# Kernel tuning notes

Hardware: AMD Instinct MI355X
Metric: run time of the kernel (lower is better)

## Reference

```python
import jax, jax.numpy as jnp
import numpy as np

K = 32          # kneighbors
HEADS = 4       # Anchor_selfattention head_num
EPS = 1e-5      # BatchNorm eps


def bn(x, gamma, beta):
    # training-mode BatchNorm1d on channel-last tensor [B, M, C]:
    # stats over batch+spatial dims per channel, biased variance (torch behavior)
    m = jnp.mean(x, axis=(0, 1), keepdims=True)
    v = jnp.var(x, axis=(0, 1), keepdims=True)
    return gamma * (x - m) * jax.lax.rsqrt(v + EPS) + beta


def setup_inputs() -> dict:
    B, NA, NP, C, NRAW = 32, 4, 16384, 256, 32768
    key = jax.random.key(0)
    ks = jax.random.split(key, 12)
    s = 0.02
    return {
        "a_points": jax.random.normal(ks[0], (B, NA, 3), jnp.float32),
        "sa_x": jax.random.normal(ks[1], (B, NP, C), jnp.float32),
        "sa_xyz": jax.random.normal(ks[2], (B, NP, 3), jnp.float32),
        "xyz_raw": jax.random.normal(ks[3], (B, NRAW, 3), jnp.float32),
        # global_layer: Conv1d(3->C, bias=False) + BN(C)
        "g_W": jax.random.normal(ks[4], (C, 3), jnp.float32) * s,
        "g_gamma": jnp.ones((C,), jnp.float32),
        "g_beta": jnp.zeros((C,), jnp.float32),
        # attention: to_qkv Linear(C -> 3C, bias=False)
        "qkv_W": jax.random.normal(ks[5], (3 * C, C), jnp.float32) * s,
        # pos_embedding: Conv1d(3->C) + BN(C)
        "pos_W": jax.random.normal(ks[6], (C, 3), jnp.float32) * s,
        "pos_b": jnp.zeros((C,), jnp.float32),
        "pos_gamma": jnp.ones((C,), jnp.float32),
        "pos_beta": jnp.zeros((C,), jnp.float32),
        # res: Conv1d(C->C) + BN(C)
        "res_W": jax.random.normal(ks[7], (C, C), jnp.float32) * s,
        "res_b": jnp.zeros((C,), jnp.float32),
        "res_gamma": jnp.ones((C,), jnp.float32),
        "res_beta": jnp.zeros((C,), jnp.float32),
        # prob_head: Conv1d(2C -> 9, bias=False) + BN(9)
        "prob_W": jax.random.normal(ks[8], (9, 2 * C), jnp.float32) * s,
        "prob_gamma": jnp.ones((9,), jnp.float32),
        "prob_beta": jnp.zeros((9,), jnp.float32),
    }


def reference(a_points, sa_x, sa_xyz, xyz_raw,
              g_W, g_gamma, g_beta,
              qkv_W,
              pos_W, pos_b, pos_gamma, pos_beta,
              res_W, res_b, res_gamma, res_beta,
              prob_W, prob_gamma, prob_beta):
    B, NA, _ = a_points.shape
    C = sa_x.shape[-1]
    hd = C // HEADS

    # ---- knn_point: squared distances anchor->points, smallest-K indices ----
    # dist[b, a, n] = |a_points[b,a] - sa_xyz[b,n]|^2
    d = (-2.0 * jnp.einsum("bac,bnc->ban", a_points, sa_xyz)
         + jnp.sum(a_points ** 2, -1)[:, :, None]
         + jnp.sum(sa_xyz ** 2, -1)[:, None, :])
    _, idx = jax.lax.top_k(-d, K)                      # [B, NA, K]

    # ---- index_points gather + max-pool over neighbors ----
    local = jnp.take_along_axis(sa_x[:, None, :, :], idx[..., None], axis=2)  # [B,NA,K,C]
    local_feat = jnp.max(local, axis=2)                # [B, NA, C]

    # ---- Anchor self-attention ----
    gc = jnp.mean(a_points, axis=1, keepdims=True)
    rel = a_points - gc                                # [B, NA, 3]
    pos = bn(rel @ pos_W.T + pos_b, pos_gamma, pos_beta)   # [B, NA, C]

    qkv = local_feat @ qkv_W.T                         # [B, NA, 3C]
    q, k, v = jnp.split(qkv, 3, axis=-1)
    q, k, v = q + pos, k + pos, v + pos
    q = q.reshape(B, NA, HEADS, hd)
    k = k.reshape(B, NA, HEADS, hd)
    v = v.reshape(B, NA, HEADS, hd)
    attn = jnp.einsum("bmhd,bnhd->bhmn", q, k) / np.sqrt(hd).astype(np.float32)
    attn = jax.nn.softmax(attn, axis=-1)
    av = jnp.einsum("bhmn,bnhd->bmhd", attn, v).reshape(B, NA, C)
    res = bn(av @ res_W.T + res_b, res_gamma, res_beta)

    local_feat = local_feat + res                      # [B, NA, C]

    # ---- global branch ----
    gfeat = bn(a_points @ g_W.T, g_gamma, g_beta)      # [B, NA, C]
    gmax = jnp.max(gfeat, axis=1, keepdims=True)       # [B, 1, C]
    feat = jnp.concatenate(
        [local_feat, jnp.broadcast_to(gmax, (B, NA, C))], axis=-1)  # [B, NA, 2C]

    prob = bn(feat @ prob_W.T, prob_gamma, prob_beta)  # [B, NA, 9]
    return prob
```

## Files before the change

### kernel.cpp

```cpp
#include <hip/hip_runtime.h>
#include <math.h>

#define NPTS 16384
#define HALF 8192
#define NB   32
#define NA   4
#define NC   256
#define KNN  32
#define NROW 128
#define CAP  1024

#define OFF_LF      0
#define OFF_QKV     32768
#define OFF_RESLIN  131072
#define OFF_POSLIN  163840
#define OFF_POSST   196608
#define OFF_GLIN    197120
#define OFF_GST     229888
#define OFF_PROBLIN 230400
#define OFF_CAND    231552
#define OFF_CNT     247936

typedef unsigned long long ull;

__global__ __launch_bounds__(512) void knn_gather_kernel(
    const float* __restrict__ a_points, const float* __restrict__ sa_xyz,
    const float* __restrict__ sa_x,
    ull* __restrict__ cand, unsigned int* __restrict__ cnt,
    float* __restrict__ lf)
{
  const int blk  = blockIdx.x;
  const int row  = blk >> 1;
  const int half = blk & 1;
  const int b    = row >> 2;
  const int t    = threadIdx.x;

  __shared__ float s_T;
  __shared__ int   s_m;
  __shared__ int   s_winflag;
  __shared__ ull   s_cand[CAP];
  __shared__ ull   s64[64];
  __shared__ int   s_top[KNN];
  __shared__ float s_lf2[2][NC];
  float* smin = (float*)s_cand;

  const float ax = a_points[row*3 + 0];
  const float ay = a_points[row*3 + 1];
  const float az = a_points[row*3 + 2];
  const float* __restrict__ xyz = sa_xyz + (size_t)b * NPTS * 3 + (size_t)half * HALF * 3;

  float d[16];
#pragma unroll
  for (int j = 0; j < 16; ++j) {
    const int n = t + 512*j;
    const float dx = xyz[n*3+0] - ax;
    const float dy = xyz[n*3+1] - ay;
    const float dz = xyz[n*3+2] - az;
    d[j] = dx*dx + dy*dy + dz*dz;
  }
  float mn = d[0];
#pragma unroll
  for (int j = 1; j < 16; ++j) mn = fminf(mn, d[j]);
  if (t == 0) s_m = 0;
  smin[t] = mn;
  __syncthreads();

  if (t < 64) {
    unsigned v[8];
#pragma unroll
    for (int q = 0; q < 8; ++q) v[q] = __float_as_uint(smin[t + 64*q]);
    unsigned lo = 0u, hi = 0x7f7fffffu;
    while (lo < hi) {
      const unsigned mid = lo + ((hi - lo) >> 1);
      int c2 = 0;
#pragma unroll
      for (int q = 0; q < 8; ++q) c2 += (int)__popcll(__ballot(v[q] <= mid));
      if (c2 >= KNN) hi = mid; else lo = mid + 1;
    }
    if (t == 0) s_T = __uint_as_float(lo);
  }
  __syncthreads();
  const float T = s_T;

#pragma unroll
  for (int j = 0; j < 16; ++j) {
    if (d[j] <= T) {
      const int pos = atomicAdd(&s_m, 1);
      if (pos < CAP)
        s_cand[pos] = ((ull)__float_as_uint(d[j]) << 32) | (unsigned)(half*HALF + t + 512*j);
    }
  }
  __syncthreads();
  const int m = (s_m < CAP) ? s_m : CAP;

  for (int c2 = t; c2 < m; c2 += 512) {
    const ull me = s_cand[c2];
    int rank = 0;
    for (int j = 0; j < m; ++j) rank += (s_cand[j] < me);
    if (rank < KNN)
      __hip_atomic_store(&cand[(size_t)row*64 + half*KNN + rank], me,
                         __ATOMIC_RELAXED, __HIP_MEMORY_SCOPE_AGENT);
  }
  __syncthreads();

  if (t == 0) {
    const unsigned old = atomicAdd(&cnt[row], 1u);
    s_winflag = (((old + 1u) & 1u) == 0u);
  }
  __syncthreads();
  if (!s_winflag) return;

  if (t < 64)
    s64[t] = __hip_atomic_load(&cand[(size_t)row*64 + t],
                               __ATOMIC_RELAXED, __HIP_MEMORY_SCOPE_AGENT);
  __syncthreads();
  if (t < 64) {
    const ull me = s64[t];
    int rank = 0;
#pragma unroll
    for (int j = 0; j < 64; ++j) rank += (s64[j] < me);
    if (rank < KNN) s_top[rank] = (int)(unsigned)(me & 0xffffffffu);
  }
  __syncthreads();

  {
    const int c = t & 255, h = t >> 8;
    const float* __restrict__ xb = sa_x + (size_t)b * NPTS * NC;
    float acc = -3.0e38f;
#pragma unroll
    for (int r2 = 0; r2 < 16; ++r2)
      acc = fmaxf(acc, xb[(size_t)s_top[h*16 + r2] * NC + c]);
    s_lf2[h][c] = acc;
  }
  __syncthreads();
  if (t < NC)
    lf[(size_t)row * NC + t] = fmaxf(s_lf2[0][t], s_lf2[1][t]);
}

__global__ __launch_bounds__(256) void lin1_kernel(
    const float* __restrict__ lf, const float* __restrict__ qkv_W,
    const float* __restrict__ a_points,
    const float* __restrict__ pos_W, const float* __restrict__ pos_b,
    const float* __restrict__ g_W,
    float* __restrict__ qkv, float* __restrict__ pos_lin, float* __restrict__ pos_stats,
    float* __restrict__ g_lin, float* __restrict__ g_stats)
{
  const int blk = blockIdx.x;
  if (blk < 96) {
    const int r0 = (blk / 12) * 16;
    const int o0 = (blk % 12) * 64;
    const int ot = threadIdx.x & 63;
    const int rt = threadIdx.x >> 6;
    const int o  = o0 + ot;
    const float* __restrict__ wrow = qkv_W + (size_t)o * NC;
    const float* __restrict__ l0p  = lf + (size_t)(r0 + rt*4) * NC;
    float acc0 = 0.f, acc1 = 0.f, acc2 = 0.f, acc3 = 0.f;
    for (int c = 0; c < NC; c += 4) {
      const float4 w4 = *(const float4*)(wrow + c);
      const float4 l0 = *(const float4*)(l0p + c);
      const float4 l1 = *(const float4*)(l0p + NC + c);
      const float4 l2 = *(const float4*)(l0p + 2*NC + c);
      const float4 l3 = *(const float4*)(l0p + 3*NC + c);
      acc0 = fmaf(l0.x,w4.x,acc0); acc0 = fmaf(l0.y,w4.y,acc0); acc0 = fmaf(l0.z,w4.z,acc0); acc0 = fmaf(l0.w,w4.w,acc0);
      acc1 = fmaf(l1.x,w4.x,acc1); acc1 = fmaf(l1.y,w4.y,acc1); acc1 = fmaf(l1.z,w4.z,acc1); acc1 = fmaf(l1.w,w4.w,acc1);
      acc2 = fmaf(l2.x,w4.x,acc2); acc2 = fmaf(l2.y,w4.y,acc2); acc2 = fmaf(l2.z,w4.z,acc2); acc2 = fmaf(l2.w,w4.w,acc2);
      acc3 = fmaf(l3.x,w4.x,acc3); acc3 = fmaf(l3.y,w4.y,acc3); acc3 = fmaf(l3.z,w4.z,acc3); acc3 = fmaf(l3.w,w4.w,acc3);
    }
    const int r = r0 + rt*4;
    qkv[(size_t)(r+0)*768 + o] = acc0;
    qkv[(size_t)(r+1)*768 + o] = acc1;
    qkv[(size_t)(r+2)*768 + o] = acc2;
    qkv[(size_t)(r+3)*768 + o] = acc3;
  } else if (blk == 96) {
    __shared__ float apts[NROW*3];
    for (int i = threadIdx.x; i < NROW*3; i += 256) apts[i] = a_points[i];
    __syncthreads();
    const int c = threadIdx.x;
    const float w0 = pos_W[c*3+0], w1 = pos_W[c*3+1], w2 = pos_W[c*3+2];
    const float bb = pos_b[c];
    float sum = 0.f, sumsq = 0.f;
    for (int b = 0; b < NB; ++b) {
      float gx=0.f, gy=0.f, gz=0.f;
#pragma unroll
      for (int a = 0; a < NA; ++a) {
        gx += apts[(b*NA+a)*3+0];
        gy += apts[(b*NA+a)*3+1];
        gz += apts[(b*NA+a)*3+2];
      }
      gx *= 0.25f; gy *= 0.25f; gz *= 0.25f;
#pragma unroll
      for (int a = 0; a < NA; ++a) {
        const float v = (apts[(b*NA+a)*3+0]-gx)*w0
                      + (apts[(b*NA+a)*3+1]-gy)*w1
                      + (apts[(b*NA+a)*3+2]-gz)*w2 + bb;
        pos_lin[(b*NA+a)*NC + c] = v;
        sum += v; sumsq += v*v;
      }
    }
    pos_stats[c] = sum; pos_stats[NC + c] = sumsq;
  } else {
    __shared__ float apts[NROW*3];
    for (int i = threadIdx.x; i < NROW*3; i += 256) apts[i] = a_points[i];
    __syncthreads();
    const int c = threadIdx.x;
    const float w0 = g_W[c*3+0], w1 = g_W[c*3+1], w2 = g_W[c*3+2];
    float sum = 0.f, sumsq = 0.f;
    for (int r = 0; r < NROW; ++r) {
      const float v = apts[r*3+0]*w0 + apts[r*3+1]*w1 + apts[r*3+2]*w2;
      g_lin[r*NC + c] = v;
      sum += v; sumsq += v*v;
    }
    g_stats[c] = sum; g_stats[NC + c] = sumsq;
  }
}

__global__ __launch_bounds__(256) void attn_kernel(
    const float* __restrict__ qkv, const float* __restrict__ pos_lin,
    const float* __restrict__ pos_stats,
    const float* __restrict__ pos_gamma, const float* __restrict__ pos_beta,
    const float* __restrict__ res_W, const float* __restrict__ res_b,
    float* __restrict__ res_lin)
{
  const int b = blockIdx.x;
  const int t = threadIdx.x;
  __shared__ float av_s[NA][NC];
  const int c = t;
  const float pmean = pos_stats[c] * (1.0f/NROW);
  const float pvar  = pos_stats[NC + c] * (1.0f/NROW) - pmean*pmean;
  const float prstd = 1.0f / sqrtf(pvar + 1e-5f);
  const float pga = pos_gamma[c], pbe = pos_beta[c];

  float q[NA], k[NA], vv[NA];
#pragma unroll
  for (int a = 0; a < NA; ++a) {
    const int row = b*NA + a;
    const float p = pga * (pos_lin[(size_t)row*NC + c] - pmean) * prstd + pbe;
    q[a]  = qkv[(size_t)row*768 +       c] + p;
    k[a]  = qkv[(size_t)row*768 + 256 + c] + p;
    vv[a] = qkv[(size_t)row*768 + 512 + c] + p;
  }
  float s[NA][NA];
#pragma unroll
  for (int m = 0; m < NA; ++m) {
#pragma unroll
    for (int n = 0; n < NA; ++n) {
      float p = q[m]*k[n];
#pragma unroll
      for (int off = 1; off < 64; off <<= 1) p += __shfl_xor(p, off);
      s[m][n] = p * 0.125f;
    }
  }
#pragma unroll
  for (int m = 0; m < NA; ++m) {
    const float mx = fmaxf(fmaxf(s[m][0], s[m][1]), fmaxf(s[m][2], s[m][3]));
    const float e0 = expf(s[m][0]-mx), e1 = expf(s[m][1]-mx);
    const float e2 = expf(s[m][2]-mx), e3 = expf(s[m][3]-mx);
    const float inv = 1.0f / (e0+e1+e2+e3);
    av_s[m][c] = (e0*vv[0] + e1*vv[1] + e2*vv[2] + e3*vv[3]) * inv;
  }
  __syncthreads();

  const float* __restrict__ wrow = res_W + (size_t)c * NC;
  float r0=0.f, r1=0.f, r2=0.f, r3=0.f;
  for (int cc = 0; cc < NC; cc += 4) {
    const float4 w4 = *(const float4*)(wrow + cc);
    const float4 v0 = *(const float4*)&av_s[0][cc];
    const float4 v1 = *(const float4*)&av_s[1][cc];
    const float4 v2 = *(const float4*)&av_s[2][cc];
    const float4 v3 = *(const float4*)&av_s[3][cc];
    r0 = fmaf(v0.x,w4.x,r0); r0 = fmaf(v0.y,w4.y,r0); r0 = fmaf(v0.z,w4.z,r0); r0 = fmaf(v0.w,w4.w,r0);
    r1 = fmaf(v1.x,w4.x,r1); r1 = fmaf(v1.y,w4.y,r1); r1 = fmaf(v1.z,w4.z,r1); r1 = fmaf(v1.w,w4.w,r1);
    r2 = fmaf(v2.x,w4.x,r2); r2 = fmaf(v2.y,w4.y,r2); r2 = fmaf(v2.z,w4.z,r2); r2 = fmaf(v2.w,w4.w,r2);
    r3 = fmaf(v3.x,w4.x,r3); r3 = fmaf(v3.y,w4.y,r3); r3 = fmaf(v3.z,w4.z,r3); r3 = fmaf(v3.w,w4.w,r3);
  }
  const float bias = res_b[c];
  res_lin[(size_t)(b*NA+0)*NC + c] = r0 + bias;
  res_lin[(size_t)(b*NA+1)*NC + c] = r1 + bias;
  res_lin[(size_t)(b*NA+2)*NC + c] = r2 + bias;
  res_lin[(size_t)(b*NA+3)*NC + c] = r3 + bias;
}

__global__ __launch_bounds__(256) void final_kernel(
    const float* __restrict__ lf, const float* __restrict__ res_lin,
    const float* __restrict__ res_gamma, const float* __restrict__ res_beta,
    const float* __restrict__ g_lin, const float* __restrict__ g_stats,
    const float* __restrict__ g_gamma, const float* __restrict__ g_beta,
    const float* __restrict__ prob_W,
    const float* __restrict__ prob_gamma, const float* __restrict__ prob_beta,
    float* __restrict__ prob_lin, unsigned int* __restrict__ cnt_out,
    float* __restrict__ out)
{
  const int b = blockIdx.x;
  const int t = threadIdx.x;
  __shared__ float feat_s[NA][2 * NC];
  __shared__ int   s_winflag;
  __shared__ float s_prob[NROW*9];
  __shared__ float pmn[9], prs[9];
  const int c = t;
  float rsum = 0.f, rss = 0.f;
#pragma unroll 16
  for (int row = 0; row < NROW; ++row) {
    const float v = res_lin[(size_t)row*NC + c];
    rsum += v; rss += v*v;
  }
  const float rmean = rsum * (1.0f/NROW);
  const float rvar  = rss * (1.0f/NROW) - rmean*rmean;
  const float rrstd = 1.0f / sqrtf(rvar + 1e-5f);
  const float rg = res_gamma[c], rb = res_beta[c];

  const float gmean = g_stats[c] * (1.0f/NROW);
  const float gvar  = g_stats[NC+c] * (1.0f/NROW) - gmean*gmean;
  const float grstd = 1.0f / sqrtf(gvar + 1e-5f);
  const float gg = g_gamma[c], gb = g_beta[c];

  float gm = -3.0e38f;
#pragma unroll
  for (int a = 0; a < NA; ++a) {
    const int row = b*NA + a;
    gm = fmaxf(gm, gg * (g_lin[(size_t)row*NC + c] - gmean) * grstd + gb);
  }
#pragma unroll
  for (int a = 0; a < NA; ++a) {
    const int row = b*NA + a;
    const float resv = rg * (res_lin[(size_t)row*NC + c] - rmean) * rrstd + rb;
    feat_s[a][c]      = lf[(size_t)row*NC + c] + resv;
    feat_s[a][NC + c] = gm;
  }
  __syncthreads();

  const int m = t >> 6, lane = t & 63;
  for (int j = 0; j < 9; ++j) {
    float p = 0.f;
#pragma unroll
    for (int k2 = 0; k2 < 8; ++k2) {
      const int cc = lane + 64*k2;
      p = fmaf(feat_s[m][cc], prob_W[j*2*NC + cc], p);
    }
#pragma unroll
    for (int off = 1; off < 64; off <<= 1) p += __shfl_xor(p, off);
    if (lane == 0)
      __hip_atomic_store(&prob_lin[(b*NA+m)*9 + j], p,
                         __ATOMIC_RELAXED, __HIP_MEMORY_SCOPE_AGENT);
  }
  __syncthreads();

  if (t == 0) {
    const unsigned old = atomicAdd(cnt_out, 1u);
    s_winflag = (((old + 1u) & 31u) == 0u);
  }
  __syncthreads();
  if (!s_winflag) return;

  for (int i = t; i < NROW*9; i += 256)
    s_prob[i] = __hip_atomic_load(&prob_lin[i], __ATOMIC_RELAXED, __HIP_MEMORY_SCOPE_AGENT);
  __syncthreads();
  if (t < 9) {
    float s = 0.f, ss = 0.f;
    for (int i = 0; i < NROW; ++i) { const float v = s_prob[i*9+t]; s += v; ss += v*v; }
    const float mm = s * (1.0f/NROW);
    const float va = ss * (1.0f/NROW) - mm*mm;
    pmn[t] = mm; prs[t] = 1.0f / sqrtf(va + 1e-5f);
  }
  __syncthreads();
  for (int i = t; i < NROW*9; i += 256) {
    const int j = i % 9;
    out[i] = prob_gamma[j] * (s_prob[i] - pmn[j]) * prs[j] + prob_beta[j];
  }
}

extern "C" void kernel_launch(void* const* d_in, const int* in_sizes, int n_in,
                              void* d_out, int out_size, void* d_ws, size_t ws_size,
                              hipStream_t stream) {
  const float* a_points  = (const float*)d_in[0];
  const float* sa_x      = (const float*)d_in[1];
  const float* sa_xyz    = (const float*)d_in[2];
  const float* g_W       = (const float*)d_in[4];
  const float* g_gamma   = (const float*)d_in[5];
  const float* g_beta    = (const float*)d_in[6];
  const float* qkv_W     = (const float*)d_in[7];
  const float* pos_W     = (const float*)d_in[8];
  const float* pos_b     = (const float*)d_in[9];
  const float* pos_gamma = (const float*)d_in[10];
  const float* pos_beta  = (const float*)d_in[11];
  const float* res_W     = (const float*)d_in[12];
  const float* res_b     = (const float*)d_in[13];
  const float* res_gamma = (const float*)d_in[14];
  const float* res_beta  = (const float*)d_in[15];
  const float* prob_W    = (const float*)d_in[16];
  const float* prob_gamma= (const float*)d_in[17];
  const float* prob_beta = (const float*)d_in[18];
  float* ws  = (float*)d_ws;
  float* out = (float*)d_out;
  unsigned int* cnt = (unsigned int*)(ws + OFF_CNT);

  knn_gather_kernel<<<256, 512, 0, stream>>>(a_points, sa_xyz, sa_x,
      (ull*)(ws + OFF_CAND), cnt, ws + OFF_LF);
  lin1_kernel<<<98, 256, 0, stream>>>(ws + OFF_LF, qkv_W, a_points, pos_W, pos_b, g_W,
      ws + OFF_QKV, ws + OFF_POSLIN, ws + OFF_POSST, ws + OFF_GLIN, ws + OFF_GST);
  attn_kernel<<<NB, 256, 0, stream>>>(ws + OFF_QKV, ws + OFF_POSLIN, ws + OFF_POSST,
      pos_gamma, pos_beta, res_W, res_b, ws + OFF_RESLIN);
  final_kernel<<<NB, 256, 0, stream>>>(ws + OFF_LF, ws + OFF_RESLIN,
      res_gamma, res_beta, ws + OFF_GLIN, ws + OFF_GST, g_gamma, g_beta,
      prob_W, prob_gamma, prob_beta,
      ws + OFF_PROBLIN, cnt + NROW, out);
}
```

Before: 57.36 us.

## Fuse post-kNN stages into one kernel with atomic-counter inter-block barriers

Merges the lin1, attention and final kernels into a single 162-block kernel. Stages are ordered by release/acquire counters that dependent blocks spin on, with counters reset inside the kNN kernel. The goal is to remove two kernel launch gaps on a tiny, latency-bound tail. The cost is spin-waiting, which relies on all 162 blocks being co-resident, and it forces atomic loads and stores on intermediate buffers.

```diff
diff --git a/kernel.cpp b/kernel.cpp
--- a/kernel.cpp
+++ b/kernel.cpp
@@ -22,6 +22,11 @@
 #define OFF_CNT     247936
 
 typedef unsigned long long ull;
+
+#define AST(p, v)  __hip_atomic_store((p), (v), __ATOMIC_RELAXED, __HIP_MEMORY_SCOPE_AGENT)
+#define ALD(p)     __hip_atomic_load((p), __ATOMIC_RELAXED, __HIP_MEMORY_SCOPE_AGENT)
+#define AINC_REL(p) __hip_atomic_fetch_add((p), 1u, __ATOMIC_RELEASE, __HIP_MEMORY_SCOPE_AGENT)
+#define ALD_ACQ(p) __hip_atomic_load((p), __ATOMIC_ACQUIRE, __HIP_MEMORY_SCOPE_AGENT)
 
 __global__ __launch_bounds__(512) void knn_gather_kernel(
     const float* __restrict__ a_points, const float* __restrict__ sa_xyz,
@@ -35,6 +40,8 @@
   const int b    = row >> 2;
   const int t    = threadIdx.x;
 
+  if (blk == 0 && t < 3) AST(&cnt[NROW + t], 0u);
+
   __shared__ float s_T;
   __shared__ int   s_m;
   __shared__ int   s_winflag;
@@ -97,9 +104,7 @@
     const ull me = s_cand[c2];
     int rank = 0;
     for (int j = 0; j < m; ++j) rank += (s_cand[j] < me);
-    if (rank < KNN)
-      __hip_atomic_store(&cand[(size_t)row*64 + half*KNN + rank], me,
-                         __ATOMIC_RELAXED, __HIP_MEMORY_SCOPE_AGENT);
+    if (rank < KNN) AST(&cand[(size_t)row*64 + half*KNN + rank], me);
   }
   __syncthreads();
 
@@ -110,9 +115,7 @@
   __syncthreads();
   if (!s_winflag) return;
 
-  if (t < 64)
-    s64[t] = __hip_atomic_load(&cand[(size_t)row*64 + t],
-                               __ATOMIC_RELAXED, __HIP_MEMORY_SCOPE_AGENT);
+  if (t < 64) s64[t] = ALD(&cand[(size_t)row*64 + t]);
   __syncthreads();
   if (t < 64) {
     const ull me = s64[t];
@@ -137,20 +140,32 @@
     lf[(size_t)row * NC + t] = fmaxf(s_lf2[0][t], s_lf2[1][t]);
 }
 
-__global__ __launch_bounds__(256) void lin1_kernel(
-    const float* __restrict__ lf, const float* __restrict__ qkv_W,
-    const float* __restrict__ a_points,
+__global__ __launch_bounds__(256) void rest_kernel(
+    const float* __restrict__ lf, const float* __restrict__ a_points,
+    const float* __restrict__ qkv_W,
     const float* __restrict__ pos_W, const float* __restrict__ pos_b,
-    const float* __restrict__ g_W,
+    const float* __restrict__ pos_gamma, const float* __restrict__ pos_beta,
+    const float* __restrict__ g_W, const float* __restrict__ g_gamma, const float* __restrict__ g_beta,
+    const float* __restrict__ res_W, const float* __restrict__ res_b,
+    const float* __restrict__ res_gamma, const float* __restrict__ res_beta,
+    const float* __restrict__ prob_W,
+    const float* __restrict__ prob_gamma, const float* __restrict__ prob_beta,
     float* __restrict__ qkv, float* __restrict__ pos_lin, float* __restrict__ pos_stats,
-    float* __restrict__ g_lin, float* __restrict__ g_stats)
+    float* __restrict__ g_lin, float* __restrict__ g_stats,
+    float* __restrict__ res_lin, float* __restrict__ prob_lin,
+    unsigned int* __restrict__ cnt, float* __restrict__ out)
 {
   const int blk = blockIdx.x;
+  const int t   = threadIdx.x;
+  unsigned int* cnt_qkv = &cnt[NROW + 0];
+  unsigned int* cnt_res = &cnt[NROW + 1];
+  unsigned int* cnt_out = &cnt[NROW + 2];
+
   if (blk < 96) {
     const int r0 = (blk / 12) * 16;
     const int o0 = (blk % 12) * 64;
-    const int ot = threadIdx.x & 63;
-    const int rt = threadIdx.x >> 6;
+    const int ot = t & 63;
+    const int rt = t >> 6;
     const int o  = o0 + ot;
     const float* __restrict__ wrow = qkv_W + (size_t)o * NC;
     const float* __restrict__ l0p  = lf + (size_t)(r0 + rt*4) * NC;
@@ -167,204 +182,205 @@
       acc3 = fmaf(l3.x,w4.x,acc3); acc3 = fmaf(l3.y,w4.y,acc3); acc3 = fmaf(l3.z,w4.z,acc3); acc3 = fmaf(l3.w,w4.w,acc3);
     }
     const int r = r0 + rt*4;
-    qkv[(size_t)(r+0)*768 + o] = acc0;
-    qkv[(size_t)(r+1)*768 + o] = acc1;
-    qkv[(size_t)(r+2)*768 + o] = acc2;
-    qkv[(size_t)(r+3)*768 + o] = acc3;
-  } else if (blk == 96) {
+    AST(&qkv[(size_t)(r+0)*768 + o], acc0);
+    AST(&qkv[(size_t)(r+1)*768 + o], acc1);
+    AST(&qkv[(size_t)(r+2)*768 + o], acc2);
+    AST(&qkv[(size_t)(r+3)*768 + o], acc3);
+    __syncthreads();
+    if (t == 0) AINC_REL(cnt_qkv);
+
+  } else if (blk < 98) {
     __shared__ float apts[NROW*3];
-    for (int i = threadIdx.x; i < NROW*3; i += 256) apts[i] = a_points[i];
-    __syncthreads();
-    const int c = threadIdx.x;
-    const float w0 = pos_W[c*3+0], w1 = pos_W[c*3+1], w2 = pos_W[c*3+2];
-    const float bb = pos_b[c];
-    float sum = 0.f, sumsq = 0.f;
-    for (int b = 0; b < NB; ++b) {
-      float gx=0.f, gy=0.f, gz=0.f;
-#pragma unroll
-      for (int a = 0; a < NA; ++a) {
-        gx += apts[(b*NA+a)*3+0];
-        gy += apts[(b*NA+a)*3+1];
-        gz += apts[(b*NA+a)*3+2];
+    for (int i = t; i < NROW*3; i += 256) apts[i] = a_points[i];
+    __syncthreads();
+    const int c = t;
+    if (blk == 96) {
+      const float w0 = pos_W[c*3+0], w1 = pos_W[c*3+1], w2 = pos_W[c*3+2];
+      const float bb = pos_b[c];
+      float sum = 0.f, sumsq = 0.f;
+      for (int b = 0; b < NB; ++b) {
+        float gx=0.f, gy=0.f, gz=0.f;
+#pragma unroll
+        for (int a = 0; a < NA; ++a) {
+          gx += apts[(b*NA+a)*3+0];
+          gy += apts[(b*NA+a)*3+1];
+          gz += apts[(b*NA+a)*3+2];
+        }
+        gx *= 0.25f; gy *= 0.25f; gz *= 0.25f;
+#pragma unroll
+        for (int a = 0; a < NA; ++a) {
+          const float v = (apts[(b*NA+a)*3+0]-gx)*w0
+                        + (apts[(b*NA+a)*3+1]-gy)*w1
+                        + (apts[(b*NA+a)*3+2]-gz)*w2 + bb;
+          AST(&pos_lin[(b*NA+a)*NC + c], v);
+          sum += v; sumsq += v*v;
+        }
       }
-      gx *= 0.25f; gy *= 0.25f; gz *= 0.25f;
-#pragma unroll
-      for (int a = 0; a < NA; ++a) {
-        const float v = (apts[(b*NA+a)*3+0]-gx)*w0
-                      + (apts[(b*NA+a)*3+1]-gy)*w1
-                      + (apts[(b*NA+a)*3+2]-gz)*w2 + bb;
-        pos_lin[(b*NA+a)*NC + c] = v;
+      AST(&pos_stats[c], sum); AST(&pos_stats[NC + c], sumsq);
+    } else {
+      const float w0 = g_W[c*3+0], w1 = g_W[c*3+1], w2 = g_W[c*3+2];
+      float sum = 0.f, sumsq = 0.f;
+      for (int r = 0; r < NROW; ++r) {
+        const float v = apts[r*3+0]*w0 + apts[r*3+1]*w1 + apts[r*3+2]*w2;
+        AST(&g_lin[r*NC + c], v);
         sum += v; sumsq += v*v;
       }
-    }
-    pos_stats[c] = sum; pos_stats[NC + c] = sumsq;
+      AST(&g_stats[c], sum); AST(&g_stats[NC + c], sumsq);
+    }
+    __syncthreads();
+    if (t == 0) AINC_REL(cnt_qkv);
+
+  } else if (blk < 130) {
+    const int b = blk - 98;
+    __shared__ float av_s[NA][NC];
+    __shared__ int s_go;
+    if (t == 0) {
+      while (ALD_ACQ(cnt_qkv) < 98u) __builtin_amdgcn_s_sleep(16);
+      s_go = 1;
+    }
+    __syncthreads();
+    (void)s_go;
+
+    const int c = t;
+    const float psum = ALD(&pos_stats[c]);
+    const float psq  = ALD(&pos_stats[NC + c]);
+    const float pmean = psum * (1.0f/NROW);
+    const float pvar  = psq * (1.0f/NROW) - pmean*pmean;
+    const float prstd = 1.0f / sqrtf(pvar + 1e-5f);
+    const float pga = pos_gamma[c], pbe = pos_beta[c];
+
+    float q[NA], k[NA], vv[NA];
+#pragma unroll
+    for (int a = 0; a < NA; ++a) {
+      const int row = b*NA + a;
+      const float p = pga * (ALD(&pos_lin[(size_t)row*NC + c]) - pmean) * prstd + pbe;
+      q[a]  = ALD(&qkv[(size_t)row*768 +       c]) + p;
+      k[a]  = ALD(&qkv[(size_t)row*768 + 256 + c]) + p;
+      vv[a] = ALD(&qkv[(size_t)row*768 + 512 + c]) + p;
+    }
+    float s[NA][NA];
+#pragma unroll
+    for (int m = 0; m < NA; ++m) {
+#pragma unroll
+      for (int n = 0; n < NA; ++n) {
+        float p = q[m]*k[n];
+#pragma unroll
+        for (int off = 1; off < 64; off <<= 1) p += __shfl_xor(p, off);
+        s[m][n] = p * 0.125f;
+      }
+    }
+#pragma unroll
+    for (int m = 0; m < NA; ++m) {
+      const float mx = fmaxf(fmaxf(s[m][0], s[m][1]), fmaxf(s[m][2], s[m][3]));
+      const float e0 = expf(s[m][0]-mx), e1 = expf(s[m][1]-mx);
+      const float e2 = expf(s[m][2]-mx), e3 = expf(s[m][3]-mx);
+      const float inv = 1.0f / (e0+e1+e2+e3);
+      av_s[m][c] = (e0*vv[0] + e1*vv[1] + e2*vv[2] + e3*vv[3]) * inv;
+    }
+    __syncthreads();
+
+    const float* __restrict__ wrow = res_W + (size_t)c * NC;
+    float r0=0.f, r1=0.f, r2=0.f, r3=0.f;
+    for (int cc = 0; cc < NC; cc += 4) {
+      const float4 w4 = *(const float4*)(wrow + cc);
+      const float4 v0 = *(const float4*)&av_s[0][cc];
+      const float4 v1 = *(const float4*)&av_s[1][cc];
+      const float4 v2 = *(const float4*)&av_s[2][cc];
+      const float4 v3 = *(const float4*)&av_s[3][cc];
+      r0 = fmaf(v0.x,w4.x,r0); r0 = fmaf(v0.y,w4.y,r0); r0 = fmaf(v0.z,w4.z,r0); r0 = fmaf(v0.w,w4.w,r0);
+      r1 = fmaf(v1.x,w4.x,r1); r1 = fmaf(v1.y,w4.y,r1); r1 = fmaf(v1.z,w4.z,r1); r1 = fmaf(v1.w,w4.w,r1);
+      r2 = fmaf(v2.x,w4.x,r2); r2 = fmaf(v2.y,w4.y,r2); r2 = fmaf(v2.z,w4.z,r2); r2 = fmaf(v2.w,w4.w,r2);
+      r3 = fmaf(v3.x,w4.x,r3); r3 = fmaf(v3.y,w4.y,r3); r3 = fmaf(v3.z,w4.z,r3); r3 = fmaf(v3.w,w4.w,r3);
+    }
+    const float bias = res_b[c];
+    AST(&res_lin[(size_t)(b*NA+0)*NC + c], r0 + bias);
+    AST(&res_lin[(size_t)(b*NA+1)*NC + c], r1 + bias);
+    AST(&res_lin[(size_t)(b*NA+2)*NC + c], r2 + bias);
+    AST(&res_lin[(size_t)(b*NA+3)*NC + c], r3 + bias);
+    __syncthreads();
+    if (t == 0) AINC_REL(cnt_res);
+
   } else {
-    __shared__ float apts[NROW*3];
-    for (int i = threadIdx.x; i < NROW*3; i += 256) apts[i] = a_points[i];
-    __syncthreads();
-    const int c = threadIdx.x;
-    const float w0 = g_W[c*3+0], w1 = g_W[c*3+1], w2 = g_W[c*3+2];
-    float sum = 0.f, sumsq = 0.f;
-    for (int r = 0; r < NROW; ++r) {
-      const float v = apts[r*3+0]*w0 + apts[r*3+1]*w1 + apts[r*3+2]*w2;
-      g_lin[r*NC + c] = v;
-      sum += v; sumsq += v*v;
-    }
-    g_stats[c] = sum; g_stats[NC + c] = sumsq;
-  }
-}
-
-__global__ __launch_bounds__(256) void attn_kernel(
-    const float* __restrict__ qkv, const float* __restrict__ pos_lin,
-    const float* __restrict__ pos_stats,
-    const float* __restrict__ pos_gamma, const float* __restrict__ pos_beta,
-    const float* __restrict__ res_W, const float* __restrict__ res_b,
-    float* __restrict__ res_lin)
-{
-  const int b = blockIdx.x;
-  const int t = threadIdx.x;
-  __shared__ float av_s[NA][NC];
-  const int c = t;
-  const float pmean = pos_stats[c] * (1.0f/NROW);
-  const float pvar  = pos_stats[NC + c] * (1.0f/NROW) - pmean*pmean;
-  const float prstd = 1.0f / sqrtf(pvar + 1e-5f);
-  const float pga = pos_gamma[c], pbe = pos_beta[c];
-
-  float q[NA], k[NA], vv[NA];
-#pragma unroll
-  for (int a = 0; a < NA; ++a) {
-    const int row = b*NA + a;
-    const float p = pga * (pos_lin[(size_t)row*NC + c] - pmean) * prstd + pbe;
-    q[a]  = qkv[(size_t)row*768 +       c] + p;
-    k[a]  = qkv[(size_t)row*768 + 256 + c] + p;
-    vv[a] = qkv[(size_t)row*768 + 512 + c] + p;
-  }
-  float s[NA][NA];
-#pragma unroll
-  for (int m = 0; m < NA; ++m) {
-#pragma unroll
-    for (int n = 0; n < NA; ++n) {
-      float p = q[m]*k[n];
+    const int b = blk - 130;
+    __shared__ float feat_s[NA][2 * NC];
+    __shared__ int   s_winflag;
+    __shared__ float s_prob[NROW*9];
+    __shared__ float pmn[9], prs[9];
+    __shared__ int s_go;
+    if (t == 0) {
+      while (ALD_ACQ(cnt_res) < 32u) __builtin_amdgcn_s_sleep(16);
+      s_go = 1;
+    }
+    __syncthreads();
+    (void)s_go;
+
+    const int c = t;
+    float rsum = 0.f, rss = 0.f;
+#pragma unroll 16
+    for (int row = 0; row < NROW; ++row) {
+      const float v = ALD(&res_lin[(size_t)row*NC + c]);
+      rsum += v; rss += v*v;
+    }
+    const float rmean = rsum * (1.0f/NROW);
+    const float rvar  = rss * (1.0f/NROW) - rmean*rmean;
+    const float rrstd = 1.0f / sqrtf(rvar + 1e-5f);
+    const float rg = res_gamma[c], rb = res_beta[c];
+
+    const float gmean = ALD(&g_stats[c]) * (1.0f/NROW);
+    const float gvar  = ALD(&g_stats[NC+c]) * (1.0f/NROW) - gmean*gmean;
+    const float grstd = 1.0f / sqrtf(gvar + 1e-5f);
+    const float gg = g_gamma[c], gb = g_beta[c];
+
+    float gm = -3.0e38f;
+#pragma unroll
+    for (int a = 0; a < NA; ++a) {
+      const int row = b*NA + a;
+      gm = fmaxf(gm, gg * (ALD(&g_lin[(size_t)row*NC + c]) - gmean) * grstd + gb);
+    }
+#pragma unroll
+    for (int a = 0; a < NA; ++a) {
+      const int row = b*NA + a;
+      const float resv = rg * (ALD(&res_lin[(size_t)row*NC + c]) - rmean) * rrstd + rb;
+      feat_s[a][c]      = lf[(size_t)row*NC + c] + resv;
+      feat_s[a][NC + c] = gm;
+    }
+    __syncthreads();
+
+    const int m = t >> 6, lane = t & 63;
+    for (int j = 0; j < 9; ++j) {
+      float p = 0.f;
+#pragma unroll
+      for (int k2 = 0; k2 < 8; ++k2) {
+        const int cc = lane + 64*k2;
+        p = fmaf(feat_s[m][cc], prob_W[j*2*NC + cc], p);
+      }
 #pragma unroll
       for (int off = 1; off < 64; off <<= 1) p += __shfl_xor(p, off);
-      s[m][n] = p * 0.125f;
-    }
-  }
-#pragma unroll
-  for (int m = 0; m < NA; ++m) {
-    const float mx = fmaxf(fmaxf(s[m][0], s[m][1]), fmaxf(s[m][2], s[m][3]));
-    const float e0 = expf(s[m][0]-mx), e1 = expf(s[m][1]-mx);
-    const float e2 = expf(s[m][2]-mx), e3 = expf(s[m][3]-mx);
-    const float inv = 1.0f / (e0+e1+e2+e3);
-    av_s[m][c] = (e0*vv[0] + e1*vv[1] + e2*vv[2] + e3*vv[3]) * inv;
-  }
-  __syncthreads();
-
-  const float* __restrict__ wrow = res_W + (size_t)c * NC;
-  float r0=0.f, r1=0.f, r2=0.f, r3=0.f;
-  for (int cc = 0; cc < NC; cc += 4) {
-    const float4 w4 = *(const float4*)(wrow + cc);
-    const float4 v0 = *(const float4*)&av_s[0][cc];
-    const float4 v1 = *(const float4*)&av_s[1][cc];
-    const float4 v2 = *(const float4*)&av_s[2][cc];
-    const float4 v3 = *(const float4*)&av_s[3][cc];
-    r0 = fmaf(v0.x,w4.x,r0); r0 = fmaf(v0.y,w4.y,r0); r0 = fmaf(v0.z,w4.z,r0); r0 = fmaf(v0.w,w4.w,r0);
-    r1 = fmaf(v1.x,w4.x,r1); r1 = fmaf(v1.y,w4.y,r1); r1 = fmaf(v1.z,w4.z,r1); r1 = fmaf(v1.w,w4.w,r1);
-    r2 = fmaf(v2.x,w4.x,r2); r2 = fmaf(v2.y,w4.y,r2); r2 = fmaf(v2.z,w4.z,r2); r2 = fmaf(v2.w,w4.w,r2);
-    r3 = fmaf(v3.x,w4.x,r3); r3 = fmaf(v3.y,w4.y,r3); r3 = fmaf(v3.z,w4.z,r3); r3 = fmaf(v3.w,w4.w,r3);
-  }
-  const float bias = res_b[c];
-  res_lin[(size_t)(b*NA+0)*NC + c] = r0 + bias;
-  res_lin[(size_t)(b*NA+1)*NC + c] = r1 + bias;
-  res_lin[(size_t)(b*NA+2)*NC + c] = r2 + bias;
-  res_lin[(size_t)(b*NA+3)*NC + c] = r3 + bias;
-}
-
-__global__ __launch_bounds__(256) void final_kernel(
-    const float* __restrict__ lf, const float* __restrict__ res_lin,
-    const float* __restrict__ res_gamma, const float* __restrict__ res_beta,
-    const float* __restrict__ g_lin, const float* __restrict__ g_stats,
-    const float* __restrict__ g_gamma, const float* __restrict__ g_beta,
-    const float* __restrict__ prob_W,
-    const float* __restrict__ prob_gamma, const float* __restrict__ prob_beta,
-    float* __restrict__ prob_lin, unsigned int* __restrict__ cnt_out,
-    float* __restrict__ out)
-{
-  const int b = blockIdx.x;
-  const int t = threadIdx.x;
-  __shared__ float feat_s[NA][2 * NC];
-  __shared__ int   s_winflag;
-  __shared__ float s_prob[NROW*9];
-  __shared__ float pmn[9], prs[9];
-  const int c = t;
-  float rsum = 0.f, rss = 0.f;
-#pragma unroll 16
-  for (int row = 0; row < NROW; ++row) {
-    const float v = res_lin[(size_t)row*NC + c];
-    rsum += v; rss += v*v;
-  }
-  const float rmean = rsum * (1.0f/NROW);
-  const float rvar  = rss * (1.0f/NROW) - rmean*rmean;
-  const float rrstd = 1.0f / sqrtf(rvar + 1e-5f);
-  const float rg = res_gamma[c], rb = res_beta[c];
-
-  const float gmean = g_stats[c] * (1.0f/NROW);
-  const float gvar  = g_stats[NC+c] * (1.0f/NROW) - gmean*gmean;
-  const float grstd = 1.0f / sqrtf(gvar + 1e-5f);
-  const float gg = g_gamma[c], gb = g_beta[c];
-
-  float gm = -3.0e38f;
-#pragma unroll
-  for (int a = 0; a < NA; ++a) {
-    const int row = b*NA + a;
-    gm = fmaxf(gm, gg * (g_lin[(size_t)row*NC + c] - gmean) * grstd + gb);
-  }
-#pragma unroll
-  for (int a = 0; a < NA; ++a) {
-    const int row = b*NA + a;
-    const float resv = rg * (res_lin[(size_t)row*NC + c] - rmean) * rrstd + rb;
-    feat_s[a][c]      = lf[(size_t)row*NC + c] + resv;
-    feat_s[a][NC + c] = gm;
-  }
-  __syncthreads();
-
-  const int m = t >> 6, lane = t & 63;
-  for (int j = 0; j < 9; ++j) {
-    float p = 0.f;
-#pragma unroll
-    for (int k2 = 0; k2 < 8; ++k2) {
-      const int cc = lane + 64*k2;
-      p = fmaf(feat_s[m][cc], prob_W[j*2*NC + cc], p);
-    }
-#pragma unroll
-    for (int off = 1; off < 64; off <<= 1) p += __shfl_xor(p, off);
-    if (lane == 0)
-      __hip_atomic_store(&prob_lin[(b*NA+m)*9 + j], p,
-                         __ATOMIC_RELAXED, __HIP_MEMORY_SCOPE_AGENT);
-  }
-  __syncthreads();
-
-  if (t == 0) {
-    const unsigned old = atomicAdd(cnt_out, 1u);
-    s_winflag = (((old + 1u) & 31u) == 0u);
-  }
-  __syncthreads();
-  if (!s_winflag) return;
-
-  for (int i = t; i < NROW*9; i += 256)
-    s_prob[i] = __hip_atomic_load(&prob_lin[i], __ATOMIC_RELAXED, __HIP_MEMORY_SCOPE_AGENT);
-  __syncthreads();
-  if (t < 9) {
-    float s = 0.f, ss = 0.f;
-    for (int i = 0; i < NROW; ++i) { const float v = s_prob[i*9+t]; s += v; ss += v*v; }
-    const float mm = s * (1.0f/NROW);
-    const float va = ss * (1.0f/NROW) - mm*mm;
-    pmn[t] = mm; prs[t] = 1.0f / sqrtf(va + 1e-5f);
-  }
-  __syncthreads();
-  for (int i = t; i < NROW*9; i += 256) {
-    const int j = i % 9;
-    out[i] = prob_gamma[j] * (s_prob[i] - pmn[j]) * prs[j] + prob_beta[j];
+      if (lane == 0) AST(&prob_lin[(b*NA+m)*9 + j], p);
+    }
+    __syncthreads();
+
+    if (t == 0) {
+      const unsigned old = AINC_REL(cnt_out);
+      s_winflag = ((old + 1u) == 32u);
+    }
+    __syncthreads();
+    if (!s_winflag) return;
+
+    for (int i = t; i < NROW*9; i += 256) s_prob[i] = ALD(&prob_lin[i]);
+    __syncthreads();
+    if (t < 9) {
+      float s = 0.f, ss = 0.f;
+      for (int i = 0; i < NROW; ++i) { const float v = s_prob[i*9+t]; s += v; ss += v*v; }
+      const float mm = s * (1.0f/NROW);
+      const float va = ss * (1.0f/NROW) - mm*mm;
+      pmn[t] = mm; prs[t] = 1.0f / sqrtf(va + 1e-5f);
+    }
+    __syncthreads();
+    for (int i = t; i < NROW*9; i += 256) {
+      const int j = i % 9;
+      out[i] = prob_gamma[j] * (s_prob[i] - pmn[j]) * prs[j] + prob_beta[j];
+    }
   }
 }
 
@@ -395,12 +411,13 @@
 
   knn_gather_kernel<<<256, 512, 0, stream>>>(a_points, sa_xyz, sa_x,
       (ull*)(ws + OFF_CAND), cnt, ws + OFF_LF);
-  lin1_kernel<<<98, 256, 0, stream>>>(ws + OFF_LF, qkv_W, a_points, pos_W, pos_b, g_W,
-      ws + OFF_QKV, ws + OFF_POSLIN, ws + OFF_POSST, ws + OFF_GLIN, ws + OFF_GST);
-  attn_kernel<<<NB, 256, 0, stream>>>(ws + OFF_QKV, ws + OFF_POSLIN, ws + OFF_POSST,
-      pos_gamma, pos_beta, res_W, res_b, ws + OFF_RESLIN);
-  final_kernel<<<NB, 256, 0, stream>>>(ws + OFF_LF, ws + OFF_RESLIN,
-      res_gamma, res_beta, ws + OFF_GLIN, ws + OFF_GST, g_gamma, g_beta,
+  rest_kernel<<<162, 256, 0, stream>>>(ws + OFF_LF, a_points, qkv_W,
+      pos_W, pos_b, pos_gamma, pos_beta,
+      g_W, g_gamma, g_beta,
+      res_W, res_b, res_gamma, res_beta,
       prob_W, prob_gamma, prob_beta,
-      ws + OFF_PROBLIN, cnt + NROW, out);
+      ws + OFF_QKV, ws + OFF_POSLIN, ws + OFF_POSST,
+      ws + OFF_GLIN, ws + OFF_GST,
+      ws + OFF_RESLIN, ws + OFF_PROBLIN,
+      cnt, out);
 }
```

Measured after the change: 65.11 us. 1.13x slower.

## Move pos/global linear blocks into knn kernel and split attention output across blocks

Applied to the files above, without the earlier changes.

The pos-embedding and global-layer linear blocks move from lin1 into two extra blocks of the knn kernel, so they overlap with the KNN search. lin1 now only runs the qkv GEMM. attn_kernel goes from 32 to 128 blocks, each computing a 64-column slice of the res linear, but every block recomputes the full attention for its batch. The final-kernel counter now resets from the knn kernel and uses an exact equality test instead of modulo.

```diff
diff --git a/kernel.cpp b/kernel.cpp
--- a/kernel.cpp
+++ b/kernel.cpp
@@ -22,18 +22,69 @@
 #define OFF_CNT     247936
 
 typedef unsigned long long ull;
+#define AST(p, v)  __hip_atomic_store((p), (v), __ATOMIC_RELAXED, __HIP_MEMORY_SCOPE_AGENT)
+#define ALD(p)     __hip_atomic_load((p), __ATOMIC_RELAXED, __HIP_MEMORY_SCOPE_AGENT)
 
 __global__ __launch_bounds__(512) void knn_gather_kernel(
     const float* __restrict__ a_points, const float* __restrict__ sa_xyz,
     const float* __restrict__ sa_x,
+    const float* __restrict__ pos_W, const float* __restrict__ pos_b,
+    const float* __restrict__ g_W,
     ull* __restrict__ cand, unsigned int* __restrict__ cnt,
-    float* __restrict__ lf)
+    float* __restrict__ lf,
+    float* __restrict__ pos_lin, float* __restrict__ pos_stats,
+    float* __restrict__ g_lin, float* __restrict__ g_stats)
 {
-  const int blk  = blockIdx.x;
+  const int blk = blockIdx.x;
+  const int t   = threadIdx.x;
+
+  if (blk >= 256) {
+    if (blk == 256 && t == 0) AST(&cnt[NROW], 0u);
+    __shared__ float apts[NROW * 3];
+    for (int i = t; i < NROW*3; i += 512) apts[i] = a_points[i];
+    __syncthreads();
+    if (t < NC) {
+      const int c = t;
+      if (blk == 256) {
+        const float w0 = pos_W[c*3+0], w1 = pos_W[c*3+1], w2 = pos_W[c*3+2];
+        const float bb = pos_b[c];
+        float sum = 0.f, sumsq = 0.f;
+        for (int b = 0; b < NB; ++b) {
+          float gx=0.f, gy=0.f, gz=0.f;
+#pragma unroll
+          for (int a = 0; a < NA; ++a) {
+            gx += apts[(b*NA+a)*3+0];
+            gy += apts[(b*NA+a)*3+1];
+            gz += apts[(b*NA+a)*3+2];
+          }
+          gx *= 0.25f; gy *= 0.25f; gz *= 0.25f;
+#pragma unroll
+          for (int a = 0; a < NA; ++a) {
+            const float v = (apts[(b*NA+a)*3+0]-gx)*w0
+                          + (apts[(b*NA+a)*3+1]-gy)*w1
+                          + (apts[(b*NA+a)*3+2]-gz)*w2 + bb;
+            pos_lin[(b*NA+a)*NC + c] = v;
+            sum += v; sumsq += v*v;
+          }
+        }
+        pos_stats[c] = sum; pos_stats[NC + c] = sumsq;
+      } else {
+        const float w0 = g_W[c*3+0], w1 = g_W[c*3+1], w2 = g_W[c*3+2];
+        float sum = 0.f, sumsq = 0.f;
+        for (int r = 0; r < NROW; ++r) {
+          const float v = apts[r*3+0]*w0 + apts[r*3+1]*w1 + apts[r*3+2]*w2;
+          g_lin[r*NC + c] = v;
+          sum += v; sumsq += v*v;
+        }
+        g_stats[c] = sum; g_stats[NC + c] = sumsq;
+      }
+    }
+    return;
+  }
+
   const int row  = blk >> 1;
   const int half = blk & 1;
   const int b    = row >> 2;
-  const int t    = threadIdx.x;
 
   __shared__ float s_T;
   __shared__ int   s_m;
@@ -97,9 +148,7 @@
     const ull me = s_cand[c2];
     int rank = 0;
     for (int j = 0; j < m; ++j) rank += (s_cand[j] < me);
-    if (rank < KNN)
-      __hip_atomic_store(&cand[(size_t)row*64 + half*KNN + rank], me,
-                         __ATOMIC_RELAXED, __HIP_MEMORY_SCOPE_AGENT);
+    if (rank < KNN) AST(&cand[(size_t)row*64 + half*KNN + rank], me);
   }
   __syncthreads();
 
@@ -110,9 +159,7 @@
   __syncthreads();
   if (!s_winflag) return;
 
-  if (t < 64)
-    s64[t] = __hip_atomic_load(&cand[(size_t)row*64 + t],
-                               __ATOMIC_RELAXED, __HIP_MEMORY_SCOPE_AGENT);
+  if (t < 64) s64[t] = ALD(&cand[(size_t)row*64 + t]);
   __syncthreads();
   if (t < 64) {
     const ull me = s64[t];
@@ -139,79 +186,33 @@
 
 __global__ __launch_bounds__(256) void lin1_kernel(
     const float* __restrict__ lf, const float* __restrict__ qkv_W,
-    const float* __restrict__ a_points,
-    const float* __restrict__ pos_W, const float* __restrict__ pos_b,
-    const float* __restrict__ g_W,
-    float* __restrict__ qkv, float* __restrict__ pos_lin, float* __restrict__ pos_stats,
-    float* __restrict__ g_lin, float* __restrict__ g_stats)
+    float* __restrict__ qkv)
 {
   const int blk = blockIdx.x;
-  if (blk < 96) {
-    const int r0 = (blk / 12) * 16;
-    const int o0 = (blk % 12) * 64;
-    const int ot = threadIdx.x & 63;
-    const int rt = threadIdx.x >> 6;
-    const int o  = o0 + ot;
-    const float* __restrict__ wrow = qkv_W + (size_t)o * NC;
-    const float* __restrict__ l0p  = lf + (size_t)(r0 + rt*4) * NC;
-    float acc0 = 0.f, acc1 = 0.f, acc2 = 0.f, acc3 = 0.f;
-    for (int c = 0; c < NC; c += 4) {
-      const float4 w4 = *(const float4*)(wrow + c);
-      const float4 l0 = *(const float4*)(l0p + c);
-      const float4 l1 = *(const float4*)(l0p + NC + c);
-      const float4 l2 = *(const float4*)(l0p + 2*NC + c);
-      const float4 l3 = *(const float4*)(l0p + 3*NC + c);
-      acc0 = fmaf(l0.x,w4.x,acc0); acc0 = fmaf(l0.y,w4.y,acc0); acc0 = fmaf(l0.z,w4.z,acc0); acc0 = fmaf(l0.w,w4.w,acc0);
-      acc1 = fmaf(l1.x,w4.x,acc1); acc1 = fmaf(l1.y,w4.y,acc1); acc1 = fmaf(l1.z,w4.z,acc1); acc1 = fmaf(l1.w,w4.w,acc1);
-      acc2 = fmaf(l2.x,w4.x,acc2); acc2 = fmaf(l2.y,w4.y,acc2); acc2 = fmaf(l2.z,w4.z,acc2); acc2 = fmaf(l2.w,w4.w,acc2);
-      acc3 = fmaf(l3.x,w4.x,acc3); acc3 = fmaf(l3.y,w4.y,acc3); acc3 = fmaf(l3.z,w4.z,acc3); acc3 = fmaf(l3.w,w4.w,acc3);
-    }
-    const int r = r0 + rt*4;
-    qkv[(size_t)(r+0)*768 + o] = acc0;
-    qkv[(size_t)(r+1)*768 + o] = acc1;
-    qkv[(size_t)(r+2)*768 + o] = acc2;
-    qkv[(size_t)(r+3)*768 + o] = acc3;
-  } else if (blk == 96) {
-    __shared__ float apts[NROW*3];
-    for (int i = threadIdx.x; i < NROW*3; i += 256) apts[i] = a_points[i];
-    __syncthreads();
-    const int c = threadIdx.x;
-    const float w0 = pos_W[c*3+0], w1 = pos_W[c*3+1], w2 = pos_W[c*3+2];
-    const float bb = pos_b[c];
-    float sum = 0.f, sumsq = 0.f;
-    for (int b = 0; b < NB; ++b) {
-      float gx=0.f, gy=0.f, gz=0.f;
-#pragma unroll
-      for (int a = 0; a < NA; ++a) {
-        gx += apts[(b*NA+a)*3+0];
-        gy += apts[(b*NA+a)*3+1];
-        gz += apts[(b*NA+a)*3+2];
-      }
-      gx *= 0.25f; gy *= 0.25f; gz *= 0.25f;
-#pragma unroll
-      for (int a = 0; a < NA; ++a) {
-        const float v = (apts[(b*NA+a)*3+0]-gx)*w0
-                      + (apts[(b*NA+a)*3+1]-gy)*w1
-                      + (apts[(b*NA+a)*3+2]-gz)*w2 + bb;
-        pos_lin[(b*NA+a)*NC + c] = v;
-        sum += v; sumsq += v*v;
-      }
-    }
-    pos_stats[c] = sum; pos_stats[NC + c] = sumsq;
-  } else {
-    __shared__ float apts[NROW*3];
-    for (int i = threadIdx.x; i < NROW*3; i += 256) apts[i] = a_points[i];
-    __syncthreads();
-    const int c = threadIdx.x;
-    const float w0 = g_W[c*3+0], w1 = g_W[c*3+1], w2 = g_W[c*3+2];
-    float sum = 0.f, sumsq = 0.f;
-    for (int r = 0; r < NROW; ++r) {
-      const float v = apts[r*3+0]*w0 + apts[r*3+1]*w1 + apts[r*3+2]*w2;
-      g_lin[r*NC + c] = v;
-      sum += v; sumsq += v*v;
-    }
-    g_stats[c] = sum; g_stats[NC + c] = sumsq;
-  }
+  const int r0 = (blk / 12) * 16;
+  const int o0 = (blk % 12) * 64;
+  const int ot = threadIdx.x & 63;
+  const int rt = threadIdx.x >> 6;
+  const int o  = o0 + ot;
+  const float* __restrict__ wrow = qkv_W + (size_t)o * NC;
+  const float* __restrict__ l0p  = lf + (size_t)(r0 + rt*4) * NC;
+  float acc0 = 0.f, acc1 = 0.f, acc2 = 0.f, acc3 = 0.f;
+  for (int c = 0; c < NC; c += 4) {
+    const float4 w4 = *(const float4*)(wrow + c);
+    const float4 l0 = *(const float4*)(l0p + c);
+    const float4 l1 = *(const float4*)(l0p + NC + c);
+    const float4 l2 = *(const float4*)(l0p + 2*NC + c);
+    const float4 l3 = *(const float4*)(l0p + 3*NC + c);
+    acc0 = fmaf(l0.x,w4.x,acc0); acc0 = fmaf(l0.y,w4.y,acc0); acc0 = fmaf(l0.z,w4.z,acc0); acc0 = fmaf(l0.w,w4.w,acc0);
+    acc1 = fmaf(l1.x,w4.x,acc1); acc1 = fmaf(l1.y,w4.y,acc1); acc1 = fmaf(l1.z,w4.z,acc1); acc1 = fmaf(l1.w,w4.w,acc1);
+    acc2 = fmaf(l2.x,w4.x,acc2); acc2 = fmaf(l2.y,w4.y,acc2); acc2 = fmaf(l2.z,w4.z,acc2); acc2 = fmaf(l2.w,w4.w,acc2);
+    acc3 = fmaf(l3.x,w4.x,acc3); acc3 = fmaf(l3.y,w4.y,acc3); acc3 = fmaf(l3.z,w4.z,acc3); acc3 = fmaf(l3.w,w4.w,acc3);
+  }
+  const int r = r0 + rt*4;
+  qkv[(size_t)(r+0)*768 + o] = acc0;
+  qkv[(size_t)(r+1)*768 + o] = acc1;
+  qkv[(size_t)(r+2)*768 + o] = acc2;
+  qkv[(size_t)(r+3)*768 + o] = acc3;
 }
 
 __global__ __launch_bounds__(256) void attn_kernel(
@@ -221,63 +222,60 @@
     const float* __restrict__ res_W, const float* __restrict__ res_b,
     float* __restrict__ res_lin)
 {
-  const int b = blockIdx.x;
-  const int t = threadIdx.x;
+  const int b  = blockIdx.x >> 2;
+  const int qo = blockIdx.x & 3;
+  const int t  = threadIdx.x;
   __shared__ float av_s[NA][NC];
-  const int c = t;
-  const float pmean = pos_stats[c] * (1.0f/NROW);
-  const float pvar  = pos_stats[NC + c] * (1.0f/NROW) - pmean*pmean;
-  const float prstd = 1.0f / sqrtf(pvar + 1e-5f);
-  const float pga = pos_gamma[c], pbe = pos_beta[c];
-
-  float q[NA], k[NA], vv[NA];
-#pragma unroll
-  for (int a = 0; a < NA; ++a) {
-    const int row = b*NA + a;
-    const float p = pga * (pos_lin[(size_t)row*NC + c] - pmean) * prstd + pbe;
-    q[a]  = qkv[(size_t)row*768 +       c] + p;
-    k[a]  = qkv[(size_t)row*768 + 256 + c] + p;
-    vv[a] = qkv[(size_t)row*768 + 512 + c] + p;
-  }
-  float s[NA][NA];
-#pragma unroll
-  for (int m = 0; m < NA; ++m) {
-#pragma unroll
-    for (int n = 0; n < NA; ++n) {
-      float p = q[m]*k[n];
-#pragma unroll
-      for (int off = 1; off < 64; off <<= 1) p += __shfl_xor(p, off);
-      s[m][n] = p * 0.125f;
-    }
-  }
-#pragma unroll
-  for (int m = 0; m < NA; ++m) {
-    const float mx = fmaxf(fmaxf(s[m][0], s[m][1]), fmaxf(s[m][2], s[m][3]));
-    const float e0 = expf(s[m][0]-mx), e1 = expf(s[m][1]-mx);
-    const float e2 = expf(s[m][2]-mx), e3 = expf(s[m][3]-mx);
-    const float inv = 1.0f / (e0+e1+e2+e3);
-    av_s[m][c] = (e0*vv[0] + e1*vv[1] + e2*vv[2] + e3*vv[3]) * inv;
-  }
-  __syncthreads();
-
-  const float* __restrict__ wrow = res_W + (size_t)c * NC;
-  float r0=0.f, r1=0.f, r2=0.f, r3=0.f;
+
+  {
+    const int c = t;
+    const float pmean = pos_stats[c] * (1.0f/NROW);
+    const float pvar  = pos_stats[NC + c] * (1.0f/NROW) - pmean*pmean;
+    const float prstd = 1.0f / sqrtf(pvar + 1e-5f);
+    const float pga = pos_gamma[c], pbe = pos_beta[c];
+
+    float q[NA], k[NA], vv[NA];
+#pragma unroll
+    for (int a = 0; a < NA; ++a) {
+      const int row = b*NA + a;
+      const float p = pga * (pos_lin[(size_t)row*NC + c] - pmean) * prstd + pbe;
+      q[a]  = qkv[(size_t)row*768 +       c] + p;
+      k[a]  = qkv[(size_t)row*768 + 256 + c] + p;
+      vv[a] = qkv[(size_t)row*768 + 512 + c] + p;
+    }
+    float s[NA][NA];
+#pragma unroll
+    for (int m = 0; m < NA; ++m) {
+#pragma unroll
+      for (int n = 0; n < NA; ++n) {
+        float p = q[m]*k[n];
+#pragma unroll
+        for (int off = 1; off < 64; off <<= 1) p += __shfl_xor(p, off);
+        s[m][n] = p * 0.125f;
+      }
+    }
+#pragma unroll
+    for (int m = 0; m < NA; ++m) {
+      const float mx = fmaxf(fmaxf(s[m][0], s[m][1]), fmaxf(s[m][2], s[m][3]));
+      const float e0 = expf(s[m][0]-mx), e1 = expf(s[m][1]-mx);
+      const float e2 = expf(s[m][2]-mx), e3 = expf(s[m][3]-mx);
+      const float inv = 1.0f / (e0+e1+e2+e3);
+      av_s[m][c] = (e0*vv[0] + e1*vv[1] + e2*vv[2] + e3*vv[3]) * inv;
+    }
+  }
+  __syncthreads();
+
+  const int ot = t & 63, rt = t >> 6;
+  const int o  = qo*64 + ot;
+  const float* __restrict__ wrow = res_W + (size_t)o * NC;
+  float acc = 0.f;
   for (int cc = 0; cc < NC; cc += 4) {
     const float4 w4 = *(const float4*)(wrow + cc);
-    const float4 v0 = *(const float4*)&av_s[0][cc];
-    const float4 v1 = *(const float4*)&av_s[1][cc];
-    const float4 v2 = *(const float4*)&av_s[2][cc];
-    const float4 v3 = *(const float4*)&av_s[3][cc];
-    r0 = fmaf(v0.x,w4.x,r0); r0 = fmaf(v0.y,w4.y,r0); r0 = fmaf(v0.z,w4.z,r0); r0 = fmaf(v0.w,w4.w,r0);
-    r1 = fmaf(v1.x,w4.x,r1); r1 = fmaf(v1.y,w4.y,r1); r1 = fmaf(v1.z,w4.z,r1); r1 = fmaf(v1.w,w4.w,r1);
-    r2 = fmaf(v2.x,w4.x,r2); r2 = fmaf(v2.y,w4.y,r2); r2 = fmaf(v2.z,w4.z,r2); r2 = fmaf(v2.w,w4.w,r2);
-    r3 = fmaf(v3.x,w4.x,r3); r3 = fmaf(v3.y,w4.y,r3); r3 = fmaf(v3.z,w4.z,r3); r3 = fmaf(v3.w,w4.w,r3);
-  }
-  const float bias = res_b[c];
-  res_lin[(size_t)(b*NA+0)*NC + c] = r0 + bias;
-  res_lin[(size_t)(b*NA+1)*NC + c] = r1 + bias;
-  res_lin[(size_t)(b*NA+2)*NC + c] = r2 + bias;
-  res_lin[(size_t)(b*NA+3)*NC + c] = r3 + bias;
+    const float4 v4 = *(const float4*)&av_s[rt][cc];
+    acc = fmaf(v4.x,w4.x,acc); acc = fmaf(v4.y,w4.y,acc);
+    acc = fmaf(v4.z,w4.z,acc); acc = fmaf(v4.w,w4.w,acc);
+  }
+  res_lin[(size_t)(b*NA+rt)*NC + o] = acc + res_b[o];
 }
 
 __global__ __launch_bounds__(256) void final_kernel(
@@ -338,21 +336,18 @@
     }
 #pragma unroll
     for (int off = 1; off < 64; off <<= 1) p += __shfl_xor(p, off);
-    if (lane == 0)
-      __hip_atomic_store(&prob_lin[(b*NA+m)*9 + j], p,
-                         __ATOMIC_RELAXED, __HIP_MEMORY_SCOPE_AGENT);
+    if (lane == 0) AST(&prob_lin[(b*NA+m)*9 + j], p);
   }
   __syncthreads();
 
   if (t == 0) {
     const unsigned old = atomicAdd(cnt_out, 1u);
-    s_winflag = (((old + 1u) & 31u) == 0u);
+    s_winflag = ((old + 1u) == 32u);
   }
   __syncthreads();
   if (!s_winflag) return;
 
-  for (int i = t; i < NROW*9; i += 256)
-    s_prob[i] = __hip_atomic_load(&prob_lin[i], __ATOMIC_RELAXED, __HIP_MEMORY_SCOPE_AGENT);
+  for (int i = t; i < NROW*9; i += 256) s_prob[i] = ALD(&prob_lin[i]);
   __syncthreads();
   if (t < 9) {
     float s = 0.f, ss = 0.f;
@@ -393,11 +388,12 @@
   float* out = (float*)d_out;
   unsigned int* cnt = (unsigned int*)(ws + OFF_CNT);
 
-  knn_gather_kernel<<<256, 512, 0, stream>>>(a_points, sa_xyz, sa_x,
-      (ull*)(ws + OFF_CAND), cnt, ws + OFF_LF);
-  lin1_kernel<<<98, 256, 0, stream>>>(ws + OFF_LF, qkv_W, a_points, pos_W, pos_b, g_W,
-      ws + OFF_QKV, ws + OFF_POSLIN, ws + OFF_POSST, ws + OFF_GLIN, ws + OFF_GST);
-  attn_kernel<<<NB, 256, 0, stream>>>(ws + OFF_QKV, ws + OFF_POSLIN, ws + OFF_POSST,
+  knn_gather_kernel<<<258, 512, 0, stream>>>(a_points, sa_xyz, sa_x,
+      pos_W, pos_b, g_W,
+      (ull*)(ws + OFF_CAND), cnt, ws + OFF_LF,
+      ws + OFF_POSLIN, ws + OFF_POSST, ws + OFF_GLIN, ws + OFF_GST);
+  lin1_kernel<<<96, 256, 0, stream>>>(ws + OFF_LF, qkv_W, ws + OFF_QKV);
+  attn_kernel<<<128, 256, 0, stream>>>(ws + OFF_QKV, ws + OFF_POSLIN, ws + OFF_POSST,
       pos_gamma, pos_beta, res_W, res_b, ws + OFF_RESLIN);
   final_kernel<<<NB, 256, 0, stream>>>(ws + OFF_LF, ws + OFF_RESLIN,
       res_gamma, res_beta, ws + OFF_GLIN, ws + OFF_GST, g_gamma, g_beta,
```

Result: no change. 57.29 us (-0.1%).
